# Performance work log

Measured on AMD Instinct MI355X. Metric: run time of the kernel, lower is better.

The kernel has to match this reference:

```python
import jax, jax.numpy as jnp
import numpy as np

PATCH = 7
STRIDE = 1
PDIM = 3 * PATCH * PATCH  # 147


def _extract_patches(im):
    # torch.nn.Unfold(kernel=7, stride=1): output [b, c*k*k, L] with channel-major
    # ordering, which matches conv_general_dilated_patches' channel-major layout.
    b = im.shape[0]
    p = jax.lax.conv_general_dilated_patches(
        im, filter_shape=(PATCH, PATCH), window_strides=(STRIDE, STRIDE), padding='VALID'
    )  # [b, 147, h', w']
    p = p.reshape(b, PDIM, -1).transpose(0, 2, 1)  # [b, L, 147]
    # normalize_patch='mean': std_mean over ALL dims, only the mean is subtracted
    return p - p.mean()


def setup_inputs() -> dict:
    key = jax.random.key(0)
    k1, k2, k3, k4, k5 = jax.random.split(key, 5)
    B, C, H, W = 16, 3, 128, 128
    L = ((H - PATCH) // STRIDE + 1) ** 2  # 14884
    n_samples, n_proj = 4096, 128
    x = jax.random.normal(k1, (B, C, H, W), dtype=jnp.float32)
    y = jax.random.normal(k2, (B, C, H, W), dtype=jnp.float32)
    # faithful quirk: sample_same_locations=True re-draws a fresh permutation for y
    idx_x = jax.random.permutation(k3, L)[:n_samples].astype(jnp.int32)
    idx_y = jax.random.permutation(k4, L)[:n_samples].astype(jnp.int32)
    proj = jax.random.normal(k5, (PDIM, n_proj), dtype=jnp.float32)
    proj = proj / jnp.linalg.norm(proj, axis=0, keepdims=True)  # unit-norm slices
    return {"x": x, "y": y, "proj": proj, "idx_x": idx_x, "idx_y": idx_y}


def reference(x, y, proj, idx_x, idx_y):
    xp = _extract_patches(x)[:, idx_x]  # [b, n, 147]
    yp = _extract_patches(y)[:, idx_y]  # [b, n, 147]
    # SWD dist_metric, vectorized over the batch dim (replaces the Python loop):
    # project patches onto random unit directions, sort along the sample axis,
    # mean absolute difference of sorted projections.
    px = jnp.sort(jnp.einsum('bnd,dp->bnp', xp, proj), axis=1)  # [b, n, P]
    py = jnp.sort(jnp.einsum('bnd,dp->bnp', yp, proj), axis=1)
    per_sample = jnp.mean(jnp.abs(px - py), axis=(1, 2))  # [b]
    return per_sample.mean()  # batch_reduction='mean'
```

## Files before the change

kernel.cpp:

```cpp
#include <hip/hip_runtime.h>
#include <cstddef>
#include <cstdint>

#define BATCH 16
#define CHAN 3
#define HH 128
#define WW 128
#define PATCHK 7
#define HP 122
#define PDIM 147
#define NSAMP 4096
#define NPROJ 128
#define IMG_PIX (CHAN*HH*WW)
#define TOT_PIX (BATCH*IMG_PIX)
#define COUNT_D ((double)BATCH*HP*HP*PDIM)

__global__ __launch_bounds__(256)
void k_wsum(const float* __restrict__ x, const float* __restrict__ y,
            double* __restrict__ outx, double* __restrict__ outy) {
  float sx = 0.f, sy = 0.f;
  const int stride = gridDim.x * blockDim.x;
  for (int e = blockIdx.x * blockDim.x + threadIdx.x; e < TOT_PIX; e += stride) {
    int j = e & (WW - 1);
    int i = (e >> 7) & (HH - 1);
    int wi = min(i, HP - 1) - max(0, i - (PATCHK - 1)) + 1;
    int wj = min(j, HP - 1) - max(0, j - (PATCHK - 1)) + 1;
    float w = (float)(wi * wj);
    sx = fmaf(x[e], w, sx);
    sy = fmaf(y[e], w, sy);
  }
  __shared__ float rx[256], ry[256];
  const int tid = threadIdx.x;
  rx[tid] = sx; ry[tid] = sy;
  __syncthreads();
  for (int off = 128; off; off >>= 1) {
    if (tid < off) { rx[tid] += rx[tid + off]; ry[tid] += ry[tid + off]; }
    __syncthreads();
  }
  if (tid == 0) { outx[blockIdx.x] = (double)rx[0]; outy[blockIdx.x] = (double)ry[0]; }
}

__global__ void k_meandiff(const double* __restrict__ px, const double* __restrict__ py,
                           double* __restrict__ dmean,
                           const float* __restrict__ proj, float* __restrict__ sp) {
  const int tid = threadIdx.x;
  if (tid < NPROJ) {
    float s = 0.f;
    for (int d = 0; d < PDIM; ++d) s += proj[d * NPROJ + tid];
    sp[tid] = s;
  }
  __shared__ double sd[256];
  sd[tid] = px[tid] - py[tid];
  __syncthreads();
  for (int off = 128; off; off >>= 1) {
    if (tid < off) sd[tid] += sd[tid + off];
    __syncthreads();
  }
  if (tid == 0) dmean[0] = sd[0] / COUNT_D;
}

#define TM 128
#define ASTR (TM + 2)

#define LB(dst, kk) _Pragma("unroll") \
  for (int pp = 0; pp < 16; ++pp) dst[pp] = bpr[(kk) * NPROJ + pp];

#define FMAK(kk, bb) { \
  const float2 a_ = *(const float2*)&As[(kk) * ASTR + lane * 2]; \
  _Pragma("unroll") \
  for (int pp = 0; pp < 16; ++pp) { \
    acc0[pp] = fmaf(a_.x, bb[pp], acc0[pp]); \
    acc1[pp] = fmaf(a_.y, bb[pp], acc1[pp]); } }

__global__ __launch_bounds__(512)
void k_proj(const float* __restrict__ x, const float* __restrict__ y,
            const float* __restrict__ proj,
            const int* __restrict__ idx_x, const int* __restrict__ idx_y,
            float* __restrict__ PX, float* __restrict__ PY) {
  __shared__ float As[PDIM * ASTR];
  __shared__ int offd[PDIM];
  __shared__ int basen[TM];

  const int z = blockIdx.z;
  const float* im = z ? y : x;
  const int* idx = z ? idx_y : idx_x;
  float* dst = z ? PY : PX;
  const int b = blockIdx.y;
  const int nbase = blockIdx.x * TM;
  const int tid = threadIdx.x;

  if (tid < PDIM) {
    int c = tid / 49, r = tid - c * 49, kh = r / 7, kw = r - kh * 7;
    offd[tid] = (c * HH + kh) * WW + kw;
  }
  if (tid >= 256 && tid < 256 + TM) {
    int n = tid - 256;
    int l = idx[nbase + n];
    int h0 = l / HP;
    basen[n] = h0 * WW + (l - h0 * HP);
  }
  __syncthreads();

  const float* imb = im + b * IMG_PIX;
  for (int q = tid; q < PDIM * TM; q += 512) {
    int d = q >> 7;
    int n = q & (TM - 1);
    As[d * ASTR + n] = imb[basen[n] + offd[d]];
  }
  __syncthreads();

  const int lane = tid & 63;
  const int w = __builtin_amdgcn_readfirstlane(tid >> 6);
  const float* bpr = proj + w * 16;

  float acc0[16], acc1[16];
#pragma unroll
  for (int pp = 0; pp < 16; ++pp) { acc0[pp] = 0.f; acc1[pp] = 0.f; }

  float b0[16], b1[16], b2[16], b3[16];
  LB(b0, 0); LB(b1, 1); LB(b2, 2);
  for (int k = 0; k < 144; k += 4) {
    LB(b3, k + 3);
    FMAK(k, b0);
    LB(b0, k + 4);
    FMAK(k + 1, b1);
    LB(b1, k + 5);
    FMAK(k + 2, b2);
    LB(b2, k + 6);
    FMAK(k + 3, b3);
  }
  FMAK(144, b0); FMAK(145, b1); FMAK(146, b2);

#pragma unroll
  for (int pp = 0; pp < 16; ++pp) {
    float* o = dst + (size_t)(b * NPROJ + w * 16 + pp) * NSAMP + nbase + lane * 2;
    *(float2*)o = make_float2(acc0[pp], acc1[pp]);
  }
}

__device__ __forceinline__ float xorf(float v, unsigned m) {
  return __int_as_float(__float_as_int(v) ^ (int)m);
}
#define CSW(a, b) { float _t = fminf(a, b); b = fmaxf(a, b); a = _t; }

#define SORT8A(v) do { \
  CSW(v[0],v[1]); CSW(v[3],v[2]); CSW(v[4],v[5]); CSW(v[7],v[6]); \
  CSW(v[0],v[2]); CSW(v[1],v[3]); CSW(v[6],v[4]); CSW(v[7],v[5]); \
  CSW(v[0],v[1]); CSW(v[2],v[3]); CSW(v[5],v[4]); CSW(v[7],v[6]); \
  CSW(v[0],v[4]); CSW(v[1],v[5]); CSW(v[2],v[6]); CSW(v[3],v[7]); \
  CSW(v[0],v[2]); CSW(v[1],v[3]); CSW(v[4],v[6]); CSW(v[5],v[7]); \
  CSW(v[0],v[1]); CSW(v[2],v[3]); CSW(v[4],v[5]); CSW(v[6],v[7]); } while (0)

#define REG3A(v) do { \
  CSW(v[0],v[4]); CSW(v[1],v[5]); CSW(v[2],v[6]); CSW(v[3],v[7]); \
  CSW(v[0],v[2]); CSW(v[1],v[3]); CSW(v[4],v[6]); CSW(v[5],v[7]); \
  CSW(v[0],v[1]); CSW(v[2],v[3]); CSW(v[4],v[5]); CSW(v[6],v[7]); } while (0)

#define FLIP8(v, m) { v[0]=xorf(v[0],m); v[1]=xorf(v[1],m); v[2]=xorf(v[2],m); \
  v[3]=xorf(v[3],m); v[4]=xorf(v[4],m); v[5]=xorf(v[5],m); v[6]=xorf(v[6],m); \
  v[7]=xorf(v[7],m); }

template <int DL>
__device__ __forceinline__ float swzxor(float v) {
  if constexpr (DL == 1) {
    return __int_as_float(
        __builtin_amdgcn_mov_dpp(__float_as_int(v), 0xB1, 0xF, 0xF, true));
  } else if constexpr (DL == 2) {
    return __int_as_float(
        __builtin_amdgcn_mov_dpp(__float_as_int(v), 0x4E, 0xF, 0xF, true));
  } else if constexpr (DL <= 16) {
    return __int_as_float(
        __builtin_amdgcn_ds_swizzle(__float_as_int(v), (DL << 10) | 0x1F));
  } else {
    return __shfl_xor(v, DL, 64);
  }
}

template <int DL>
__device__ __forceinline__ void shufxy(float (&vx)[8], float (&vy)[8], bool keepLo) {
#pragma unroll
  for (int r = 0; r < 8; ++r) {
    float ox = swzxor<DL>(vx[r]);
    vx[r] = keepLo ? fminf(vx[r], ox) : fmaxf(vx[r], ox);
    float oy = swzxor<DL>(vy[r]);
    vy[r] = keepLo ? fminf(vy[r], oy) : fmaxf(vy[r], oy);
  }
}

__device__ __forceinline__ void lds_stage(float (&vx)[8], float (&vy)[8],
                                          float* lx, float* ly, int t, int dl, bool kl) {
  ((float4*)lx)[t * 2]     = make_float4(vx[0], vx[1], vx[2], vx[3]);
  ((float4*)lx)[t * 2 + 1] = make_float4(vx[4], vx[5], vx[6], vx[7]);
  ((float4*)ly)[t * 2]     = make_float4(vy[0], vy[1], vy[2], vy[3]);
  ((float4*)ly)[t * 2 + 1] = make_float4(vy[4], vy[5], vy[6], vy[7]);
  __syncthreads();
  const int pt = (t ^ dl) * 2;
  float4 ox0 = ((const float4*)lx)[pt], ox1 = ((const float4*)lx)[pt + 1];
  float4 oy0 = ((const float4*)ly)[pt], oy1 = ((const float4*)ly)[pt + 1];
  vx[0] = kl ? fminf(vx[0], ox0.x) : fmaxf(vx[0], ox0.x);
  vx[1] = kl ? fminf(vx[1], ox0.y) : fmaxf(vx[1], ox0.y);
  vx[2] = kl ? fminf(vx[2], ox0.z) : fmaxf(vx[2], ox0.z);
  vx[3] = kl ? fminf(vx[3], ox0.w) : fmaxf(vx[3], ox0.w);
  vx[4] = kl ? fminf(vx[4], ox1.x) : fmaxf(vx[4], ox1.x);
  vx[5] = kl ? fminf(vx[5], ox1.y) : fmaxf(vx[5], ox1.y);
  vx[6] = kl ? fminf(vx[6], ox1.z) : fmaxf(vx[6], ox1.z);
  vx[7] = kl ? fminf(vx[7], ox1.w) : fmaxf(vx[7], ox1.w);
  vy[0] = kl ? fminf(vy[0], oy0.x) : fmaxf(vy[0], oy0.x);
  vy[1] = kl ? fminf(vy[1], oy0.y) : fmaxf(vy[1], oy0.y);
  vy[2] = kl ? fminf(vy[2], oy0.z) : fmaxf(vy[2], oy0.z);
  vy[3] = kl ? fminf(vy[3], oy0.w) : fmaxf(vy[3], oy0.w);
  vy[4] = kl ? fminf(vy[4], oy1.x) : fmaxf(vy[4], oy1.x);
  vy[5] = kl ? fminf(vy[5], oy1.y) : fmaxf(vy[5], oy1.y);
  vy[6] = kl ? fminf(vy[6], oy1.z) : fmaxf(vy[6], oy1.z);
  vy[7] = kl ? fminf(vy[7], oy1.w) : fmaxf(vy[7], oy1.w);
  __syncthreads();
}

__global__ __launch_bounds__(512)
void k_sortdiff(const float* __restrict__ PX, const float* __restrict__ PY,
                const float* __restrict__ sp, const double* __restrict__ dmean,
                float* __restrict__ bsum) {
  __shared__ float lx[NSAMP];
  __shared__ float ly[NSAMP];
  __shared__ float red[8];
  const int bp = blockIdx.x;
  const int p = bp & (NPROJ - 1);
  const unsigned t = threadIdx.x;

  const unsigned g = t ^ (t >> 1);
  const unsigned mA    = (t & 1u)   << 31;
  const unsigned dA16  = (g & 1u)   << 31;
  const unsigned d16   = (g & 2u)   << 30;
  const unsigned d32   = (g & 4u)   << 29;
  const unsigned d64   = (g & 8u)   << 28;
  const unsigned d128  = (g & 16u)  << 27;
  const unsigned d256  = (g & 32u)  << 26;
  const unsigned d512  = (g & 64u)  << 25;
  const unsigned d1024 = (g & 128u) << 24;
  const unsigned d2048 = (t & 256u) << 23;

  const bool k1  = (t & 1u)  == 0, k2  = (t & 2u)  == 0, k4 = (t & 4u) == 0;
  const bool k8  = (t & 8u)  == 0, k16 = (t & 16u) == 0, k32 = (t & 32u) == 0;
  const bool kl64 = (t & 64u) == 0, kl128 = (t & 128u) == 0, kl256 = (t & 256u) == 0;

  float vx[8], vy[8];
  {
    const float4* rx = (const float4*)(PX + (size_t)bp * NSAMP) + t * 2;
    const float4* ry = (const float4*)(PY + (size_t)bp * NSAMP) + t * 2;
    float4 x0 = rx[0], x1 = rx[1], y0 = ry[0], y1 = ry[1];
    vx[0]=x0.x; vx[1]=x0.y; vx[2]=x0.z; vx[3]=x0.w;
    vx[4]=x1.x; vx[5]=x1.y; vx[6]=x1.z; vx[7]=x1.w;
    vy[0]=y0.x; vy[1]=y0.y; vy[2]=y0.z; vy[3]=y0.w;
    vy[4]=y1.x; vy[5]=y1.y; vy[6]=y1.z; vy[7]=y1.w;
  }

  FLIP8(vx, mA); FLIP8(vy, mA);
  SORT8A(vx); SORT8A(vy);
  FLIP8(vx, dA16); FLIP8(vy, dA16);

  shufxy<1>(vx, vy, k1); REG3A(vx); REG3A(vy);
  FLIP8(vx, d16); FLIP8(vy, d16);
  shufxy<2>(vx, vy, k2); shufxy<1>(vx, vy, k1); REG3A(vx); REG3A(vy);
  FLIP8(vx, d32); FLIP8(vy, d32);
  shufxy<4>(vx, vy, k4); shufxy<2>(vx, vy, k2); shufxy<1>(vx, vy, k1);
  REG3A(vx); REG3A(vy);
  FLIP8(vx, d64); FLIP8(vy, d64);
  shufxy<8>(vx, vy, k8); shufxy<4>(vx, vy, k4); shufxy<2>(vx, vy, k2);
  shufxy<1>(vx, vy, k1); REG3A(vx); REG3A(vy);
  FLIP8(vx, d128); FLIP8(vy, d128);
  shufxy<16>(vx, vy, k16); shufxy<8>(vx, vy, k8); shufxy<4>(vx, vy, k4);
  shufxy<2>(vx, vy, k2); shufxy<1>(vx, vy, k1); REG3A(vx); REG3A(vy);
  FLIP8(vx, d256); FLIP8(vy, d256);
  shufxy<32>(vx, vy, k32); shufxy<16>(vx, vy, k16); shufxy<8>(vx, vy, k8);
  shufxy<4>(vx, vy, k4); shufxy<2>(vx, vy, k2); shufxy<1>(vx, vy, k1);
  REG3A(vx); REG3A(vy);
  FLIP8(vx, d512); FLIP8(vy, d512);
  lds_stage(vx, vy, lx, ly, (int)t, 64, kl64);
  shufxy<32>(vx, vy, k32); shufxy<16>(vx, vy, k16); shufxy<8>(vx, vy, k8);
  shufxy<4>(vx, vy, k4); shufxy<2>(vx, vy, k2); shufxy<1>(vx, vy, k1);
  REG3A(vx); REG3A(vy);
  FLIP8(vx, d1024); FLIP8(vy, d1024);
  lds_stage(vx, vy, lx, ly, (int)t, 128, kl128);
  lds_stage(vx, vy, lx, ly, (int)t, 64, kl64);
  shufxy<32>(vx, vy, k32); shufxy<16>(vx, vy, k16); shufxy<8>(vx, vy, k8);
  shufxy<4>(vx, vy, k4); shufxy<2>(vx, vy, k2); shufxy<1>(vx, vy, k1);
  REG3A(vx); REG3A(vy);
  FLIP8(vx, d2048); FLIP8(vy, d2048);
  lds_stage(vx, vy, lx, ly, (int)t, 256, kl256);
  lds_stage(vx, vy, lx, ly, (int)t, 128, kl128);
  lds_stage(vx, vy, lx, ly, (int)t, 64, kl64);
  shufxy<32>(vx, vy, k32); shufxy<16>(vx, vy, k16); shufxy<8>(vx, vy, k8);
  shufxy<4>(vx, vy, k4); shufxy<2>(vx, vy, k2); shufxy<1>(vx, vy, k1);
  REG3A(vx); REG3A(vy);

  const float delta = (float)(dmean[0]) * sp[p];
  float s = 0.f;
#pragma unroll
  for (int r = 0; r < 8; ++r) s += fabsf(vx[r] - vy[r] - delta);

#pragma unroll
  for (int o = 1; o < 64; o <<= 1) s += __shfl_xor(s, o, 64);
  if ((t & 63u) == 0) red[t >> 6] = s;
  __syncthreads();
  if (t == 0) {
    float tot = 0.f;
#pragma unroll
    for (int i = 0; i < 8; ++i) tot += red[i];
    bsum[bp] = tot;
  }
}

__global__ void k_final(const float* __restrict__ bsum, float* __restrict__ out) {
  __shared__ double s[256];
  const int tid = threadIdx.x;
  double v = 0.0;
  for (int q = tid; q < BATCH * NPROJ; q += 256) v += (double)bsum[q];
  s[tid] = v;
  __syncthreads();
  for (int off = 128; off; off >>= 1) {
    if (tid < off) s[tid] += s[tid + off];
    __syncthreads();
  }
  if (tid == 0) out[0] = (float)(s[0] / ((double)NSAMP * NPROJ * BATCH));
}

extern "C" void kernel_launch(void* const* d_in, const int* in_sizes, int n_in,
                              void* d_out, int out_size, void* d_ws, size_t ws_size,
                              hipStream_t stream) {
  const float* x    = (const float*)d_in[0];
  const float* y    = (const float*)d_in[1];
  const float* proj = (const float*)d_in[2];
  const int* idx_x  = (const int*)d_in[3];
  const int* idx_y  = (const int*)d_in[4];
  float* out = (float*)d_out;

  char* ws = (char*)d_ws;
  double* pAx   = (double*)(ws + 0);
  double* pAy   = (double*)(ws + 2048);
  double* dmean = (double*)(ws + 4096);
  float*  sp    = (float*)(ws + 4160);
  float*  bsum  = (float*)(ws + 8192);
  float*  PX    = (float*)(ws + 16384);
  float*  PY    = PX + (size_t)BATCH * NPROJ * NSAMP;

  const size_t need = 16384 + 2ull * BATCH * NPROJ * NSAMP * sizeof(float);
  if (ws_size < need) return;

  k_wsum    <<<256, 256, 0, stream>>>(x, y, pAx, pAy);
  k_meandiff<<<1, 256, 0, stream>>>(pAx, pAy, dmean, proj, sp);
  k_proj    <<<dim3(NSAMP / TM, BATCH, 2), 512, 0, stream>>>(x, y, proj, idx_x, idx_y, PX, PY);
  k_sortdiff<<<BATCH * NPROJ, 512, 0, stream>>>(PX, PY, sp, dmean, bsum);
  k_final   <<<1, 256, 0, stream>>>(bsum, out);
}
```

Measured before the change: 245.8 us.

## Split projection K dimension into two LDS phases to shrink shared memory

The projection kernel now stages the gathered patch matrix in two halves of 74 rows instead of all 147 rows. This halves the LDS footprint so more blocks can be resident, and a launch-bounds occupancy hint is added. The gather loop is reordered so consecutive threads walk the patch dimension within one sample, and the padded row is zero-filled. The cost is an extra barrier plus some clamped redundant proj loads, and the new gather order may coalesce global reads less well.

```diff
diff --git a/kernel.cpp b/kernel.cpp
--- a/kernel.cpp
+++ b/kernel.cpp
@@ -61,6 +61,8 @@
 
 #define TM 128
 #define ASTR (TM + 2)
+#define KROWS 74
+#define MINK(v) ((v) < 146 ? (v) : 146)
 
 #define LB(dst, kk) _Pragma("unroll") \
   for (int pp = 0; pp < 16; ++pp) dst[pp] = bpr[(kk) * NPROJ + pp];
@@ -72,12 +74,12 @@
     acc0[pp] = fmaf(a_.x, bb[pp], acc0[pp]); \
     acc1[pp] = fmaf(a_.y, bb[pp], acc1[pp]); } }
 
-__global__ __launch_bounds__(512)
+__global__ __launch_bounds__(512, 8)
 void k_proj(const float* __restrict__ x, const float* __restrict__ y,
             const float* __restrict__ proj,
             const int* __restrict__ idx_x, const int* __restrict__ idx_y,
             float* __restrict__ PX, float* __restrict__ PY) {
-  __shared__ float As[PDIM * ASTR];
+  __shared__ float As[KROWS * ASTR];
   __shared__ int offd[PDIM];
   __shared__ int basen[TM];
 
@@ -102,13 +104,6 @@
   __syncthreads();
 
   const float* imb = im + b * IMG_PIX;
-  for (int q = tid; q < PDIM * TM; q += 512) {
-    int d = q >> 7;
-    int n = q & (TM - 1);
-    As[d * ASTR + n] = imb[basen[n] + offd[d]];
-  }
-  __syncthreads();
-
   const int lane = tid & 63;
   const int w = __builtin_amdgcn_readfirstlane(tid >> 6);
   const float* bpr = proj + w * 16;
@@ -117,19 +112,34 @@
 #pragma unroll
   for (int pp = 0; pp < 16; ++pp) { acc0[pp] = 0.f; acc1[pp] = 0.f; }
 
-  float b0[16], b1[16], b2[16], b3[16];
-  LB(b0, 0); LB(b1, 1); LB(b2, 2);
-  for (int k = 0; k < 144; k += 4) {
-    LB(b3, k + 3);
-    FMAK(k, b0);
-    LB(b0, k + 4);
-    FMAK(k + 1, b1);
-    LB(b1, k + 5);
-    FMAK(k + 2, b2);
-    LB(b2, k + 6);
-    FMAK(k + 3, b3);
-  }
-  FMAK(144, b0); FMAK(145, b1); FMAK(146, b2);
+#pragma unroll 1
+  for (int ph = 0; ph < 2; ++ph) {
+    const int k0 = ph ? KROWS : 0;
+    if (ph) __syncthreads();
+
+    for (int e = tid; e < KROWS * TM; e += 512) {
+      int n = e / KROWS;
+      int dr = e - n * KROWS;
+      int d = dr + k0;
+      As[dr * ASTR + n] = (d < PDIM) ? imb[basen[n] + offd[d]] : 0.f;
+    }
+    __syncthreads();
+
+    float b0[16], b1[16], b2[16], b3[16];
+    LB(b0, k0); LB(b1, k0 + 1); LB(b2, k0 + 2);
+    for (int kk = 0; kk < 72; kk += 4) {
+      LB(b3, MINK(k0 + kk + 3));
+      FMAK(kk, b0);
+      LB(b0, MINK(k0 + kk + 4));
+      FMAK(kk + 1, b1);
+      LB(b1, MINK(k0 + kk + 5));
+      FMAK(kk + 2, b2);
+      LB(b2, MINK(k0 + kk + 6));
+      FMAK(kk + 3, b3);
+    }
+    FMAK(72, b0);
+    FMAK(73, b1);
+  }
 
 #pragma unroll
   for (int pp = 0; pp < 16; ++pp) {
```

New measurement: 226.2 us. 1.09x faster.
